# Optimization experiments

Measured on AMD Instinct MI355X. Metric: run time of the kernel, lower is better.

## Reference

```python
import jax, jax.numpy as jnp
import numpy as np

LRELU = 0.2
EPS_LN = 1e-5
EPS_BN = 1e-5


def _seg_softmax(logits, seg, n):
    # softmax over edges grouped by destination node (PyG softmax), logits [E,H]
    m = jax.ops.segment_max(logits, seg, num_segments=n)
    e = jnp.exp(logits - m[seg])
    s = jax.ops.segment_sum(e, seg, num_segments=n)
    return e / (s[seg] + 1e-16)


def _gat(x, src, dst, n, W, a_src, a_dst, b, H, C):
    # PyG GATConv, concat=False (mean over heads), leaky_relu slope 0.2
    h = (x @ W).reshape(n, H, C)
    e = (h * a_src).sum(-1)[src] + (h * a_dst).sum(-1)[dst]  # [E,H]
    e = jnp.where(e > 0, e, LRELU * e)
    alpha = _seg_softmax(e, dst, n)
    out = jax.ops.segment_sum(h[src] * alpha[:, :, None], dst, num_segments=n)  # [N,H,C]
    return out.mean(1) + b


def _gcn(x, src, dst, n, W, b):
    # PyG GCNConv with symmetric normalization; edge list already contains self loops
    deg = jax.ops.segment_sum(jnp.ones(src.shape, x.dtype), dst, num_segments=n)
    dis = jnp.where(deg > 0, jax.lax.rsqrt(jnp.maximum(deg, 1e-12)), 0.0)
    h = x @ W
    w = (dis[src] * dis[dst])[:, None]
    return jax.ops.segment_sum(h[src] * w, dst, num_segments=n) + b


def _ln(x, g, b):
    mu = x.mean(-1, keepdims=True)
    v = x.var(-1, keepdims=True)
    return (x - mu) * jax.lax.rsqrt(v + EPS_LN) * g + b


def _bn_eval(x, g, b, rm, rv):
    return (x - rm) * jax.lax.rsqrt(rv + EPS_BN) * g + b


def _forward(x, edge_index, gin, bti, rmi, rvi, W1, as1, ad1, b1, Wg1, bg1,
             W2, as2, ad2, b2, Wg2, bg2, Ws, bs, Wf, bf,
             g1, be1, g2, be2, g3, be3, Wc1, bc1, gbn, bbn, rmb, rvb, Wc2, bc2):
    n = x.shape[0]
    xn = _bn_eval(x, gin, bti, rmi, rvi)
    sl = jnp.arange(n, dtype=edge_index.dtype)
    src = jnp.concatenate([edge_index[0], sl])
    dst = jnp.concatenate([edge_index[1], sl])
    # GAT1 (4 heads, 128) -> LN -> relu
    x1 = _gat(xn, src, dst, n, W1, as1, ad1, b1, 4, 128)
    x1 = jax.nn.relu(_ln(x1, g1, be1))
    # GCN1 -> relu
    x1g = jax.nn.relu(_gcn(x1, src, dst, n, Wg1, bg1))
    # GAT2 (2 heads, 64) -> LN -> relu
    x2 = _gat(x1g, src, dst, n, W2, as2, ad2, b2, 2, 64)
    x2 = jax.nn.relu(_ln(x2, g2, be2))
    # GCN2 -> relu
    x2g = jax.nn.relu(_gcn(x2, src, dst, n, Wg2, bg2))
    # skip + fusion
    skip = jax.nn.relu(xn @ Ws + bs)
    fused = jax.nn.relu(jnp.concatenate([x1g, x2g], axis=1) @ Wf + bf)
    final = _ln(fused + skip, g3, be3)
    # classifier: Linear -> BN(eval) -> relu -> Linear
    h = jax.nn.relu(_bn_eval(final @ Wc1 + bc1, gbn, bbn, rmb, rvb))
    return h @ Wc2 + bc2


def setup_inputs():
    key = jax.random.key(0)
    ks = jax.random.split(key, 20)
    N, F, E = 20000, 512, 160000
    H1, C1, H2, C2 = 4, 128, 2, 64
    rn = lambda k, sh, s=0.05: (jax.random.normal(k, sh) * s).astype(jnp.float32)
    return dict(
        x=jax.random.normal(ks[0], (N, F), jnp.float32),
        edge_index=jax.random.randint(ks[1], (2, E), 0, N, jnp.int32),
        gin=jnp.ones((F,), jnp.float32), bti=jnp.zeros((F,), jnp.float32),
        rmi=rn(ks[2], (F,)), rvi=(jax.random.uniform(ks[3], (F,)) + 0.5).astype(jnp.float32),
        W1=rn(ks[4], (F, H1 * C1)), as1=rn(ks[5], (H1, C1)), ad1=rn(ks[6], (H1, C1)), b1=jnp.zeros((C1,), jnp.float32),
        Wg1=rn(ks[7], (C1, C1)), bg1=jnp.zeros((C1,), jnp.float32),
        W2=rn(ks[8], (C1, H2 * C2)), as2=rn(ks[9], (H2, C2)), ad2=rn(ks[10], (H2, C2)), b2=jnp.zeros((C2,), jnp.float32),
        Wg2=rn(ks[11], (C2, C2)), bg2=jnp.zeros((C2,), jnp.float32),
        Ws=rn(ks[12], (F, C2)), bs=jnp.zeros((C2,), jnp.float32),
        Wf=rn(ks[13], (C1 + C2, C2)), bf=jnp.zeros((C2,), jnp.float32),
        g1=jnp.ones((C1,), jnp.float32), be1=jnp.zeros((C1,), jnp.float32),
        g2=jnp.ones((C2,), jnp.float32), be2=jnp.zeros((C2,), jnp.float32),
        g3=jnp.ones((C2,), jnp.float32), be3=jnp.zeros((C2,), jnp.float32),
        Wc1=rn(ks[14], (C2, 32)), bc1=jnp.zeros((32,), jnp.float32),
        gbn=jnp.ones((32,), jnp.float32), bbn=jnp.zeros((32,), jnp.float32),
        rmb=rn(ks[15], (32,)), rvb=(jax.random.uniform(ks[16], (32,)) + 0.5).astype(jnp.float32),
        Wc2=rn(ks[17], (32, 5)), bc2=jnp.zeros((5,), jnp.float32),
    )


def reference(x, edge_index, gin, bti, rmi, rvi, W1, as1, ad1, b1, Wg1, bg1,
              W2, as2, ad2, b2, Wg2, bg2, Ws, bs, Wf, bf,
              g1, be1, g2, be2, g3, be3, Wc1, bc1, gbn, bbn, rmb, rvb, Wc2, bc2):
    return _forward(x, edge_index, gin, bti, rmi, rvi, W1, as1, ad1, b1, Wg1, bg1,
                    W2, as2, ad2, b2, Wg2, bg2, Ws, bs, Wf, bf,
                    g1, be1, g2, be2, g3, be3, Wc1, bc1, gbn, bbn, rmb, rvb, Wc2, bc2)
```

## Files before the change

kernel.cpp:

```cpp
#include <hip/hip_runtime.h>
#include <hip/hip_bf16.h>

#define N_NODES 20000
#define F_IN 512

typedef __attribute__((ext_vector_type(8))) short short8;
typedef __attribute__((ext_vector_type(4))) float f32x4;

__device__ __forceinline__ ushort f2bf(float f) {
    uint u = __float_as_uint(f);
    u += 0x7FFF + ((u >> 16) & 1);
    return (ushort)(u >> 16);
}
__device__ __forceinline__ float bf2f(ushort h) { return __uint_as_float((uint)h << 16); }

__device__ __forceinline__ void gload_lds16(const void* g, void* l) {
    __builtin_amdgcn_global_load_lds(
        (const __attribute__((address_space(1))) void*)g,
        (__attribute__((address_space(3))) void*)l, 16, 0, 0);
}

__global__ void zero_int_k(int* p, int n) {
    int i = blockIdx.x * blockDim.x + threadIdx.x;
    if (i < n) p[i] = 0;
}

__global__ void hist_k(const int* __restrict__ ei, int E0, int N, int* __restrict__ deg) {
    int e = blockIdx.x * blockDim.x + threadIdx.x;
    int Etot = E0 + N;
    if (e >= Etot) return;
    int dst = (e < E0) ? ei[E0 + e] : (e - E0);
    atomicAdd(&deg[dst], 1);
}

__global__ __launch_bounds__(1024) void scan_k(const int* __restrict__ deg, int* __restrict__ rp,
                                               int* __restrict__ fp, float* __restrict__ dis,
                                               int N, int Etot) {
    __shared__ int part[1024];
    int tid = threadIdx.x;
    int chunk = (N + 1023) / 1024;
    int lo = tid * chunk, hi = min(lo + chunk, N);
    int s = 0;
    for (int i = lo; i < hi; i++) s += deg[i];
    part[tid] = s;
    __syncthreads();
    for (int off = 1; off < 1024; off <<= 1) {
        int t = 0;
        if (tid >= off) t = part[tid - off];
        __syncthreads();
        part[tid] += t;
        __syncthreads();
    }
    int run = part[tid] - s;
    for (int i = lo; i < hi; i++) {
        rp[i] = run; fp[i] = run;
        int d = deg[i];
        dis[i] = (d > 0) ? rsqrtf((float)d) : 0.f;
        run += d;
    }
    if (tid == 1023) { rp[N] = Etot; fp[N] = Etot; }
}

__global__ void scatter_k(const int* __restrict__ ei, int E0, int N, int* __restrict__ fp,
                          int* __restrict__ csr_src) {
    int e = blockIdx.x * blockDim.x + threadIdx.x;
    int Etot = E0 + N;
    if (e >= Etot) return;
    int src, dst;
    if (e < E0) { src = ei[e]; dst = ei[E0 + e]; }
    else        { src = e - E0; dst = src; }
    int pos = atomicAdd(&fp[dst], 1);
    csr_src[pos] = src;
}

__global__ void bnprep_k(const float* __restrict__ g, const float* __restrict__ b,
                         const float* __restrict__ rm, const float* __restrict__ rv,
                         float* __restrict__ sc, float* __restrict__ sh, int n) {
    int i = blockIdx.x * blockDim.x + threadIdx.x;
    if (i >= n) return;
    float s = g[i] * rsqrtf(rv[i] + 1e-5f);
    sc[i] = s;
    sh[i] = b[i] - rm[i] * s;
}

__global__ void splitA_k(const float* __restrict__ x, const float* __restrict__ sc,
                         const float* __restrict__ sh, ushort* __restrict__ Ah,
                         ushort* __restrict__ Al, int M, int Mpad) {
    size_t i4 = (size_t)blockIdx.x * blockDim.x + threadIdx.x;
    size_t base = i4 * 4;
    if (base >= (size_t)Mpad * 512) return;
    int row = (int)(base >> 9);
    ushort4 ah = {0, 0, 0, 0}, al = {0, 0, 0, 0};
    if (row < M) {
        float4 v = *(const float4*)&x[base];
        int c = (int)(base & 511);
        float f0 = v.x * sc[c] + sh[c];
        float f1 = v.y * sc[c + 1] + sh[c + 1];
        float f2 = v.z * sc[c + 2] + sh[c + 2];
        float f3 = v.w * sc[c + 3] + sh[c + 3];
        ah.x = f2bf(f0); al.x = f2bf(f0 - bf2f(ah.x));
        ah.y = f2bf(f1); al.y = f2bf(f1 - bf2f(ah.y));
        ah.z = f2bf(f2); al.z = f2bf(f2 - bf2f(ah.z));
        ah.w = f2bf(f3); al.w = f2bf(f3 - bf2f(ah.w));
    }
    *(ushort4*)&Ah[base] = ah;
    *(ushort4*)&Al[base] = al;
}

__global__ __launch_bounds__(256) void splitBt_k(const float* __restrict__ W1, const float* __restrict__ Ws,
                                                 ushort* __restrict__ Bth, ushort* __restrict__ Btl) {
    __shared__ float tile[64][65];
    int n0 = blockIdx.x * 64;
    int k0 = blockIdx.y * 64;
    int t = threadIdx.x;
    int a = t >> 6, b = t & 63;
#pragma unroll
    for (int i = 0; i < 16; i++) {
        int kk = a + i * 4, nn = b;
        int gk = k0 + kk, gn = n0 + nn;
        float v;
        if (gn < 512)      v = W1[(size_t)gk * 512 + gn];
        else if (gn < 576) v = Ws[(size_t)gk * 64 + (gn - 512)];
        else               v = 0.f;
        tile[kk][nn] = v;
    }
    __syncthreads();
#pragma unroll
    for (int i = 0; i < 16; i++) {
        int nn = a + i * 4, kk = b;
        float v = tile[kk][nn];
        ushort hi = f2bf(v);
        ushort lo = f2bf(v - bf2f(hi));
        Bth[(size_t)(n0 + nn) * 512 + k0 + kk] = hi;
        Btl[(size_t)(n0 + nn) * 512 + k0 + kk] = lo;
    }
}

__global__ __launch_bounds__(256) void mfma_gemm_k(
    const ushort* __restrict__ Ah, const ushort* __restrict__ Al,
    const ushort* __restrict__ Bth, const ushort* __restrict__ Btl,
    const float* __restrict__ bs, float* __restrict__ h1, float* __restrict__ skip,
    int M, int K) {
    __shared__ ushort Ah_s[128 * 32];
    __shared__ ushort Al_s[128 * 32];
    __shared__ ushort Bh_s[128 * 32];
    __shared__ ushort Bl_s[128 * 32];
    int t = threadIdx.x;
    int w = t >> 6, l = t & 63;
    int bm = blockIdx.y * 128;
    int n0 = blockIdx.x * 128;
    int r0 = (w & 1) * 64, c0 = (w >> 1) * 64;

    f32x4 acc[4][4] = {};

    int elem0 = t * 8;
    int rowS = elem0 >> 5, kofs = elem0 & 31;
    const size_t aoff1 = (size_t)(bm + rowS) * 512 + kofs;
    const size_t aoff2 = (size_t)(bm + rowS + 64) * 512 + kofs;
    const size_t boff1 = (size_t)(n0 + rowS) * 512 + kofs;
    const size_t boff2 = (size_t)(n0 + rowS + 64) * 512 + kofs;

    for (int kt = 0; kt < K; kt += 32) {
        gload_lds16(Ah + aoff1 + kt, &Ah_s[elem0]);
        gload_lds16(Ah + aoff2 + kt, &Ah_s[elem0 + 2048]);
        gload_lds16(Al + aoff1 + kt, &Al_s[elem0]);
        gload_lds16(Al + aoff2 + kt, &Al_s[elem0 + 2048]);
        gload_lds16(Bth + boff1 + kt, &Bh_s[elem0]);
        gload_lds16(Bth + boff2 + kt, &Bh_s[elem0 + 2048]);
        gload_lds16(Btl + boff1 + kt, &Bl_s[elem0]);
        gload_lds16(Btl + boff2 + kt, &Bl_s[elem0 + 2048]);
        __syncthreads();

        short8 ah[4], al4[4], bh[4], bl[4];
        int kg = (l >> 4) * 8;
        int lr = l & 15;
#pragma unroll
        for (int f = 0; f < 4; f++) {
            int ra = (r0 + f * 16 + lr) * 32 + kg;
            ah[f]  = *(const short8*)&Ah_s[ra];
            al4[f] = *(const short8*)&Al_s[ra];
            int rb = (c0 + f * 16 + lr) * 32 + kg;
            bh[f] = *(const short8*)&Bh_s[rb];
            bl[f] = *(const short8*)&Bl_s[rb];
        }
#pragma unroll
        for (int fm = 0; fm < 4; fm++)
#pragma unroll
            for (int fn = 0; fn < 4; fn++) {
                acc[fm][fn] = __builtin_amdgcn_mfma_f32_16x16x32_bf16(ah[fm], bh[fn], acc[fm][fn], 0, 0, 0);
                acc[fm][fn] = __builtin_amdgcn_mfma_f32_16x16x32_bf16(ah[fm], bl[fn], acc[fm][fn], 0, 0, 0);
                acc[fm][fn] = __builtin_amdgcn_mfma_f32_16x16x32_bf16(al4[fm], bh[fn], acc[fm][fn], 0, 0, 0);
            }
        __syncthreads();
    }

#pragma unroll
    for (int fm = 0; fm < 4; fm++) {
        int row_base = bm + r0 + fm * 16 + (l >> 4) * 4;
#pragma unroll
        for (int fn = 0; fn < 4; fn++) {
            int col = n0 + c0 + fn * 16 + (l & 15);
#pragma unroll
            for (int r = 0; r < 4; r++) {
                int row = row_base + r;
                if (row < M) {
                    float v = acc[fm][fn][r];
                    if (col < 512) h1[(size_t)row * 512 + col] = v;
                    else if (col < 576) skip[(size_t)row * 64 + (col - 512)] = fmaxf(v + bs[col - 512], 0.f);
                }
            }
        }
    }
}

template <int K, int NOUT>
__global__ __launch_bounds__(NOUT) void rowgemm_k(const float* __restrict__ X, const float* __restrict__ W,
                                                  float* __restrict__ out, int N) {
    __shared__ float Ws[K * NOUT];
    __shared__ float Xs[4][K];
    int c = threadIdx.x;
    for (int i = c; i < K * NOUT; i += NOUT) Ws[i] = W[i];
    for (int r0 = blockIdx.x * 4; r0 < N; r0 += gridDim.x * 4) {
        int nr = min(4, N - r0);
        __syncthreads();
        for (int i = c; i < nr * K; i += NOUT) Xs[i / K][i % K] = X[(size_t)r0 * K + i];
        __syncthreads();
        float acc[4] = {0.f, 0.f, 0.f, 0.f};
        for (int k = 0; k < K; k++) {
            float w = Ws[k * NOUT + c];
#pragma unroll
            for (int r = 0; r < 4; r++) acc[r] += Xs[r][k] * w;
        }
        for (int r = 0; r < nr; r++) out[(size_t)(r0 + r) * NOUT + c] = acc[r];
    }
}

template <int H, int C>
__global__ __launch_bounds__(256) void scores_k(const float* __restrict__ h, const float* __restrict__ a_src,
                                                const float* __restrict__ a_dst, float* __restrict__ ss,
                                                float* __restrict__ sd, int N) {
    int wid = (blockIdx.x * blockDim.x + threadIdx.x) >> 6;
    int lane = threadIdx.x & 63;
    if (wid >= N * H) return;
    int hh = wid % H;
    const float* hp = h + (size_t)(wid / H) * (H * C) + hh * C;
    float s1 = 0.f, s2 = 0.f;
    for (int c = lane; c < C; c += 64) {
        float v = hp[c];
        s1 += v * a_src[hh * C + c];
        s2 += v * a_dst[hh * C + c];
    }
#pragma unroll
    for (int off = 32; off; off >>= 1) {
        s1 += __shfl_down(s1, off);
        s2 += __shfl_down(s2, off);
    }
    if (lane == 0) { ss[wid] = s1; sd[wid] = s2; }
}

template <int H, int C>
__global__ __launch_bounds__(C) void gat_agg_k(const float* __restrict__ h, const float* __restrict__ ss,
                                               const float* __restrict__ sd, const float* __restrict__ bias,
                                               const float* __restrict__ g, const float* __restrict__ be,
                                               const int* __restrict__ rp, const int* __restrict__ csr_src,
                                               float* __restrict__ out, int N) {
    int n = blockIdx.x;
    int tid = threadIdx.x;
    __shared__ float m_s[H], s_s[H];
    __shared__ int srcs[64];
    __shared__ float aw[64 * H];
    int e0 = rp[n], deg = rp[n + 1] - e0;

    if (tid < H) {
        float m = -1e30f, s = 0.f;
        float sdv = sd[n * H + tid];
        for (int k = 0; k < deg; k++) {
            int src = csr_src[e0 + k];
            float e = ss[src * H + tid] + sdv;
            e = (e > 0.f) ? e : 0.2f * e;
            float mn = fmaxf(m, e);
            s = s * __expf(m - mn) + __expf(e - mn);
            m = mn;
        }
        m_s[tid] = m;
        s_s[tid] = s + 1e-16f;
    }
    __syncthreads();

    float acc = 0.f;
    for (int t0 = 0; t0 < deg; t0 += 64) {
        int tl = min(64, deg - t0);
        if (tid < tl) srcs[tid] = csr_src[e0 + t0 + tid];
        __syncthreads();
        for (int idx = tid; idx < tl * H; idx += C) {
            int k = idx / H, hh = idx % H;
            int src = srcs[k];
            float e = ss[src * H + hh] + sd[n * H + hh];
            e = (e > 0.f) ? e : 0.2f * e;
            aw[idx] = __expf(e - m_s[hh]) / s_s[hh];
        }
        __syncthreads();
        for (int k = 0; k < tl; k++) {
            const float* hp = h + (size_t)srcs[k] * (H * C) + tid;
#pragma unroll
            for (int hh = 0; hh < H; hh++) acc += aw[k * H + hh] * hp[hh * C];
        }
        __syncthreads();
    }

    float v = acc * (1.f / H) + bias[tid];
    float* r1 = aw;
    r1[tid] = v;
    __syncthreads();
    for (int s = C / 2; s > 0; s >>= 1) {
        if (tid < s) r1[tid] += r1[tid + s];
        __syncthreads();
    }
    float mu = r1[0] * (1.f / C);
    __syncthreads();
    float d = v - mu;
    r1[tid] = d * d;
    __syncthreads();
    for (int s = C / 2; s > 0; s >>= 1) {
        if (tid < s) r1[tid] += r1[tid + s];
        __syncthreads();
    }
    float var = r1[0] * (1.f / C);
    float y = d * rsqrtf(var + 1e-5f) * g[tid] + be[tid];
    out[(size_t)n * C + tid] = fmaxf(y, 0.f);
}

template <int C>
__global__ __launch_bounds__(C) void gcn_agg_k(const float* __restrict__ h, const float* __restrict__ dis,
                                               const float* __restrict__ bias, const int* __restrict__ rp,
                                               const int* __restrict__ csr_src, float* __restrict__ out, int N) {
    int n = blockIdx.x;
    int tid = threadIdx.x;
    __shared__ int srcs[64];
    __shared__ float w[64];
    int e0 = rp[n], deg = rp[n + 1] - e0;
    float dn = dis[n];
    float acc = 0.f;
    for (int t0 = 0; t0 < deg; t0 += 64) {
        int tl = min(64, deg - t0);
        if (tid < tl) {
            int s = csr_src[e0 + t0 + tid];
            srcs[tid] = s;
            w[tid] = dis[s] * dn;
        }
        __syncthreads();
        for (int k = 0; k < tl; k++) acc += w[k] * h[(size_t)srcs[k] * C + tid];
        __syncthreads();
    }
    out[(size_t)n * C + tid] = fmaxf(acc + bias[tid], 0.f);
}

__global__ __launch_bounds__(64) void fusion_k(const float* __restrict__ x1g, const float* __restrict__ x2g,
                                               const float* __restrict__ Wf, const float* __restrict__ bf,
                                               const float* __restrict__ skip, const float* __restrict__ g3,
                                               const float* __restrict__ be3, float* __restrict__ fin, int N) {
    int n = blockIdx.x;
    int c = threadIdx.x;
    __shared__ float cat[192];
    cat[c] = x1g[(size_t)n * 128 + c];
    cat[64 + c] = x1g[(size_t)n * 128 + 64 + c];
    cat[128 + c] = x2g[(size_t)n * 64 + c];
    __syncthreads();
    float acc = bf[c];
    for (int j = 0; j < 192; j++) acc += cat[j] * Wf[j * 64 + c];
    acc = fmaxf(acc, 0.f) + skip[(size_t)n * 64 + c];
    float mu = acc;
#pragma unroll
    for (int off = 32; off; off >>= 1) mu += __shfl_xor(mu, off);
    mu *= (1.f / 64.f);
    float d = acc - mu;
    float var = d * d;
#pragma unroll
    for (int off = 32; off; off >>= 1) var += __shfl_xor(var, off);
    var *= (1.f / 64.f);
    fin[(size_t)n * 64 + c] = d * rsqrtf(var + 1e-5f) * g3[c] + be3[c];
}

__global__ __launch_bounds__(64) void classifier_k(const float* __restrict__ fin, const float* __restrict__ Wc1,
                                                   const float* __restrict__ bc1, const float* __restrict__ gbn,
                                                   const float* __restrict__ bbn, const float* __restrict__ rmb,
                                                   const float* __restrict__ rvb, const float* __restrict__ Wc2,
                                                   const float* __restrict__ bc2, float* __restrict__ out, int N) {
    int n = blockIdx.x;
    int t = threadIdx.x;
    __shared__ float f[64];
    __shared__ float hbuf[32];
    f[t] = fin[(size_t)n * 64 + t];
    __syncthreads();
    if (t < 32) {
        float acc = bc1[t];
        for (int j = 0; j < 64; j++) acc += f[j] * Wc1[j * 32 + t];
        acc = (acc - rmb[t]) * rsqrtf(rvb[t] + 1e-5f) * gbn[t] + bbn[t];
        hbuf[t] = fmaxf(acc, 0.f);
    }
    __syncthreads();
    if (t < 5) {
        float acc = bc2[t];
        for (int j = 0; j < 32; j++) acc += hbuf[j] * Wc2[j * 5 + t];
        out[(size_t)n * 5 + t] = acc;
    }
}

extern "C" void kernel_launch(void* const* d_in, const int* in_sizes, int n_in,
                              void* d_out, int out_size, void* d_ws, size_t ws_size,
                              hipStream_t stream) {
    const float* x   = (const float*)d_in[0];
    const int*   ei  = (const int*)d_in[1];
    const float* gin = (const float*)d_in[2];
    const float* bti = (const float*)d_in[3];
    const float* rmi = (const float*)d_in[4];
    const float* rvi = (const float*)d_in[5];
    const float* W1  = (const float*)d_in[6];
    const float* as1 = (const float*)d_in[7];
    const float* ad1 = (const float*)d_in[8];
    const float* b1  = (const float*)d_in[9];
    const float* Wg1 = (const float*)d_in[10];
    const float* bg1 = (const float*)d_in[11];
    const float* W2  = (const float*)d_in[12];
    const float* as2 = (const float*)d_in[13];
    const float* ad2 = (const float*)d_in[14];
    const float* b2  = (const float*)d_in[15];
    const float* Wg2 = (const float*)d_in[16];
    const float* bg2 = (const float*)d_in[17];
    const float* Ws  = (const float*)d_in[18];
    const float* bs  = (const float*)d_in[19];
    const float* Wf  = (const float*)d_in[20];
    const float* bf  = (const float*)d_in[21];
    const float* g1  = (const float*)d_in[22];
    const float* be1 = (const float*)d_in[23];
    const float* g2  = (const float*)d_in[24];
    const float* be2 = (const float*)d_in[25];
    const float* g3  = (const float*)d_in[26];
    const float* be3 = (const float*)d_in[27];
    const float* Wc1 = (const float*)d_in[28];
    const float* bc1 = (const float*)d_in[29];
    const float* gbn = (const float*)d_in[30];
    const float* bbn = (const float*)d_in[31];
    const float* rmb = (const float*)d_in[32];
    const float* rvb = (const float*)d_in[33];
    const float* Wc2 = (const float*)d_in[34];
    const float* bc2 = (const float*)d_in[35];
    float* out = (float*)d_out;

    const int N = in_sizes[0] / F_IN;
    const int E0 = in_sizes[1] / 2;
    const int Etot = E0 + N;
    const int Mpad = 20096;

    char* wp = (char*)d_ws;
    auto alloc = [&](size_t bytes) -> void* {
        void* p = (void*)wp;
        wp += (bytes + 255) & ~(size_t)255;
        return p;
    };
    float* h1   = (float*)alloc((size_t)N * 512 * 4);
    ushort* Ah  = (ushort*)alloc((size_t)Mpad * 512 * 2);
    ushort* Al  = (ushort*)alloc((size_t)Mpad * 512 * 2);
    ushort* Bth = (ushort*)alloc((size_t)640 * 512 * 2);
    ushort* Btl = (ushort*)alloc((size_t)640 * 512 * 2);
    float* skip = (float*)alloc((size_t)N * 64 * 4);
    float* ss1  = (float*)alloc((size_t)N * 4 * 4);
    float* sd1  = (float*)alloc((size_t)N * 4 * 4);
    float* ss2  = (float*)alloc((size_t)N * 2 * 4);
    float* sd2  = (float*)alloc((size_t)N * 2 * 4);
    float* dis  = (float*)alloc((size_t)N * 4);
    float* sc   = (float*)alloc((size_t)F_IN * 4);
    float* sh   = (float*)alloc((size_t)F_IN * 4);
    int* deg    = (int*)alloc((size_t)N * 4);
    int* rp     = (int*)alloc((size_t)(N + 1) * 4);
    int* fp     = (int*)alloc((size_t)(N + 1) * 4);
    int* csr    = (int*)alloc((size_t)Etot * 4);
    float* hg1 = h1;
    float* x1g = h1 + (size_t)N * 128;
    float* h2  = h1 + (size_t)N * 256;
    float* x2  = h1 + (size_t)N * 384;
    float* hg2 = h1 + (size_t)N * 448;
    float* x1  = (float*)Ah;
    float* x2g = x1 + (size_t)N * 128;
    float* fin = x2g + (size_t)N * 64;

    zero_int_k<<<(N + 255) / 256, 256, 0, stream>>>(deg, N);
    hist_k<<<(Etot + 255) / 256, 256, 0, stream>>>(ei, E0, N, deg);
    scan_k<<<1, 1024, 0, stream>>>(deg, rp, fp, dis, N, Etot);
    scatter_k<<<(Etot + 255) / 256, 256, 0, stream>>>(ei, E0, N, fp, csr);
    bnprep_k<<<2, 256, 0, stream>>>(gin, bti, rmi, rvi, sc, sh, F_IN);
    splitA_k<<<(int)(((size_t)Mpad * 512 / 4 + 255) / 256), 256, 0, stream>>>(x, sc, sh, Ah, Al, N, Mpad);
    splitBt_k<<<dim3(10, 8), 256, 0, stream>>>(W1, Ws, Bth, Btl);

    mfma_gemm_k<<<dim3(5, 157), 256, 0, stream>>>(Ah, Al, Bth, Btl, bs, h1, skip, N, 512);

    scores_k<4, 128><<<(N * 4 + 3) / 4, 256, 0, stream>>>(h1, as1, ad1, ss1, sd1, N);
    gat_agg_k<4, 128><<<N, 128, 0, stream>>>(h1, ss1, sd1, b1, g1, be1, rp, csr, x1, N);

    rowgemm_k<128, 128><<<512, 128, 0, stream>>>(x1, Wg1, hg1, N);
    gcn_agg_k<128><<<N, 128, 0, stream>>>(hg1, dis, bg1, rp, csr, x1g, N);

    rowgemm_k<128, 128><<<512, 128, 0, stream>>>(x1g, W2, h2, N);
    scores_k<2, 64><<<(N * 2 + 3) / 4, 256, 0, stream>>>(h2, as2, ad2, ss2, sd2, N);
    gat_agg_k<2, 64><<<N, 64, 0, stream>>>(h2, ss2, sd2, b2, g2, be2, rp, csr, x2, N);

    rowgemm_k<64, 64><<<512, 64, 0, stream>>>(x2, Wg2, hg2, N);
    gcn_agg_k<64><<<N, 64, 0, stream>>>(hg2, dis, bg2, rp, csr, x2g, N);

    fusion_k<<<N, 64, 0, stream>>>(x1g, x2g, Wf, bf, skip, g3, be3, fin, N);

    classifier_k<<<N, 64, 0, stream>>>(fin, Wc1, bc1, gbn, bbn, rmb, rvb, Wc2, bc2, out, N);
}
```

Measured before the change: 583.8 us.

## Remap GEMM grid across XCDs, parallelize GAT softmax, fuse tail kernels

Several independent changes land together. The MFMA GEMM now uses a 1D grid that is remapped so neighbouring tiles land on the same XCD, and its LDS layout moves to k-group-major. rowgemm processes 8 rows per block and is launched on more blocks. GAT aggregation computes the online softmax with 32 lanes per head instead of one thread per head, caches edge logits in shared memory for small degrees, and does the LayerNorm with shuffles instead of a shared-memory tree. The final GCN aggregation, fusion and classifier are merged into one kernel, which removes intermediate buffers and launches but puts more work in each block.

```diff
diff --git a/kernel.cpp b/kernel.cpp
--- a/kernel.cpp
+++ b/kernel.cpp
@@ -147,39 +147,46 @@
     __shared__ ushort Bl_s[128 * 32];
     int t = threadIdx.x;
     int w = t >> 6, l = t & 63;
-    int bm = blockIdx.y * 128;
-    int n0 = blockIdx.x * 128;
+
+    int nwg = gridDim.x;
+    int q = nwg >> 3, r = nwg & 7;
+    int xcd = blockIdx.x & 7, lid = blockIdx.x >> 3;
+    int wg = (xcd < r) ? xcd * (q + 1) + lid : r * (q + 1) + (xcd - r) * q + lid;
+    int by = wg / 5, bx = wg % 5;
+    int bm = by * 128;
+    int n0 = bx * 128;
     int r0 = (w & 1) * 64, c0 = (w >> 1) * 64;
 
     f32x4 acc[4][4] = {};
 
+    int kg_t = t >> 7;
+    int row_t = t & 127;
+    const size_t ga1 = (size_t)(bm + row_t) * 512 + kg_t * 8;
+    const size_t ga2 = (size_t)(bm + row_t) * 512 + (kg_t + 2) * 8;
+    const size_t gb1 = (size_t)(n0 + row_t) * 512 + kg_t * 8;
+    const size_t gb2 = (size_t)(n0 + row_t) * 512 + (kg_t + 2) * 8;
     int elem0 = t * 8;
-    int rowS = elem0 >> 5, kofs = elem0 & 31;
-    const size_t aoff1 = (size_t)(bm + rowS) * 512 + kofs;
-    const size_t aoff2 = (size_t)(bm + rowS + 64) * 512 + kofs;
-    const size_t boff1 = (size_t)(n0 + rowS) * 512 + kofs;
-    const size_t boff2 = (size_t)(n0 + rowS + 64) * 512 + kofs;
 
     for (int kt = 0; kt < K; kt += 32) {
-        gload_lds16(Ah + aoff1 + kt, &Ah_s[elem0]);
-        gload_lds16(Ah + aoff2 + kt, &Ah_s[elem0 + 2048]);
-        gload_lds16(Al + aoff1 + kt, &Al_s[elem0]);
-        gload_lds16(Al + aoff2 + kt, &Al_s[elem0 + 2048]);
-        gload_lds16(Bth + boff1 + kt, &Bh_s[elem0]);
-        gload_lds16(Bth + boff2 + kt, &Bh_s[elem0 + 2048]);
-        gload_lds16(Btl + boff1 + kt, &Bl_s[elem0]);
-        gload_lds16(Btl + boff2 + kt, &Bl_s[elem0 + 2048]);
+        gload_lds16(Ah + ga1 + kt, &Ah_s[elem0]);
+        gload_lds16(Ah + ga2 + kt, &Ah_s[elem0 + 2048]);
+        gload_lds16(Al + ga1 + kt, &Al_s[elem0]);
+        gload_lds16(Al + ga2 + kt, &Al_s[elem0 + 2048]);
+        gload_lds16(Bth + gb1 + kt, &Bh_s[elem0]);
+        gload_lds16(Bth + gb2 + kt, &Bh_s[elem0 + 2048]);
+        gload_lds16(Btl + gb1 + kt, &Bl_s[elem0]);
+        gload_lds16(Btl + gb2 + kt, &Bl_s[elem0 + 2048]);
         __syncthreads();
 
         short8 ah[4], al4[4], bh[4], bl[4];
-        int kg = (l >> 4) * 8;
+        int kgl = l >> 4;
         int lr = l & 15;
 #pragma unroll
         for (int f = 0; f < 4; f++) {
-            int ra = (r0 + f * 16 + lr) * 32 + kg;
+            int ra = kgl * 1024 + (r0 + f * 16 + lr) * 8;
             ah[f]  = *(const short8*)&Ah_s[ra];
             al4[f] = *(const short8*)&Al_s[ra];
-            int rb = (c0 + f * 16 + lr) * 32 + kg;
+            int rb = kgl * 1024 + (c0 + f * 16 + lr) * 8;
             bh[f] = *(const short8*)&Bh_s[rb];
             bl[f] = *(const short8*)&Bl_s[rb];
         }
@@ -201,10 +208,10 @@
         for (int fn = 0; fn < 4; fn++) {
             int col = n0 + c0 + fn * 16 + (l & 15);
 #pragma unroll
-            for (int r = 0; r < 4; r++) {
-                int row = row_base + r;
+            for (int r2 = 0; r2 < 4; r2++) {
+                int row = row_base + r2;
                 if (row < M) {
-                    float v = acc[fm][fn][r];
+                    float v = acc[fm][fn][r2];
                     if (col < 512) h1[(size_t)row * 512 + col] = v;
                     else if (col < 576) skip[(size_t)row * 64 + (col - 512)] = fmaxf(v + bs[col - 512], 0.f);
                 }
@@ -217,19 +224,19 @@
 __global__ __launch_bounds__(NOUT) void rowgemm_k(const float* __restrict__ X, const float* __restrict__ W,
                                                   float* __restrict__ out, int N) {
     __shared__ float Ws[K * NOUT];
-    __shared__ float Xs[4][K];
+    __shared__ float Xs[8][K];
     int c = threadIdx.x;
     for (int i = c; i < K * NOUT; i += NOUT) Ws[i] = W[i];
-    for (int r0 = blockIdx.x * 4; r0 < N; r0 += gridDim.x * 4) {
-        int nr = min(4, N - r0);
+    for (int r0 = blockIdx.x * 8; r0 < N; r0 += gridDim.x * 8) {
+        int nr = min(8, N - r0);
         __syncthreads();
         for (int i = c; i < nr * K; i += NOUT) Xs[i / K][i % K] = X[(size_t)r0 * K + i];
         __syncthreads();
-        float acc[4] = {0.f, 0.f, 0.f, 0.f};
+        float acc[8] = {};
         for (int k = 0; k < K; k++) {
             float w = Ws[k * NOUT + c];
 #pragma unroll
-            for (int r = 0; r < 4; r++) acc[r] += Xs[r][k] * w;
+            for (int r = 0; r < 8; r++) acc[r] += Xs[r][k] * w;
         }
         for (int r = 0; r < nr; r++) out[(size_t)(r0 + r) * NOUT + c] = acc[r];
     }
@@ -266,66 +273,94 @@
                                                float* __restrict__ out, int N) {
     int n = blockIdx.x;
     int tid = threadIdx.x;
-    __shared__ float m_s[H], s_s[H];
+    __shared__ float m_s[H], s_s[H], red[4];
     __shared__ int srcs[64];
     __shared__ float aw[64 * H];
     int e0 = rp[n], deg = rp[n + 1] - e0;
-
-    if (tid < H) {
-        float m = -1e30f, s = 0.f;
-        float sdv = sd[n * H + tid];
+    bool small = (deg <= 64);
+    int hh = tid >> 5, l = tid & 31;
+
+    if (small && tid < deg) srcs[tid] = csr_src[e0 + tid];
+    __syncthreads();
+
+    float sdv = sd[n * H + hh];
+    float m = -1e30f, s = 0.f;
+    for (int k = l; k < deg; k += 32) {
+        int src = small ? srcs[k] : csr_src[e0 + k];
+        float e = ss[src * H + hh] + sdv;
+        e = (e > 0.f) ? e : 0.2f * e;
+        if (small) aw[k * H + hh] = e;
+        float mn = fmaxf(m, e);
+        s = s * __expf(m - mn) + __expf(e - mn);
+        m = mn;
+    }
+#pragma unroll
+    for (int off = 16; off; off >>= 1) {
+        float mo = __shfl_xor(m, off), so = __shfl_xor(s, off);
+        float mn = fmaxf(m, mo);
+        s = s * __expf(m - mn) + so * __expf(mo - mn);
+        m = mn;
+    }
+    if (l == 0) { m_s[hh] = m; s_s[hh] = s + 1e-16f; }
+    __syncthreads();
+
+    float v = 0.f;
+    if (small) {
+        for (int idx = tid; idx < deg * H; idx += C) {
+            int h2 = idx & (H - 1);
+            aw[idx] = __expf(aw[idx] - m_s[h2]) / s_s[h2];
+        }
+        __syncthreads();
         for (int k = 0; k < deg; k++) {
-            int src = csr_src[e0 + k];
-            float e = ss[src * H + tid] + sdv;
-            e = (e > 0.f) ? e : 0.2f * e;
-            float mn = fmaxf(m, e);
-            s = s * __expf(m - mn) + __expf(e - mn);
-            m = mn;
-        }
-        m_s[tid] = m;
-        s_s[tid] = s + 1e-16f;
-    }
-    __syncthreads();
-
-    float acc = 0.f;
-    for (int t0 = 0; t0 < deg; t0 += 64) {
-        int tl = min(64, deg - t0);
-        if (tid < tl) srcs[tid] = csr_src[e0 + t0 + tid];
-        __syncthreads();
-        for (int idx = tid; idx < tl * H; idx += C) {
-            int k = idx / H, hh = idx % H;
-            int src = srcs[k];
-            float e = ss[src * H + hh] + sd[n * H + hh];
-            e = (e > 0.f) ? e : 0.2f * e;
-            aw[idx] = __expf(e - m_s[hh]) / s_s[hh];
-        }
-        __syncthreads();
-        for (int k = 0; k < tl; k++) {
             const float* hp = h + (size_t)srcs[k] * (H * C) + tid;
 #pragma unroll
-            for (int hh = 0; hh < H; hh++) acc += aw[k * H + hh] * hp[hh * C];
-        }
-        __syncthreads();
-    }
-
-    float v = acc * (1.f / H) + bias[tid];
-    float* r1 = aw;
-    r1[tid] = v;
-    __syncthreads();
-    for (int s = C / 2; s > 0; s >>= 1) {
-        if (tid < s) r1[tid] += r1[tid + s];
-        __syncthreads();
-    }
-    float mu = r1[0] * (1.f / C);
-    __syncthreads();
+            for (int h2 = 0; h2 < H; h2++) v += aw[k * H + h2] * hp[h2 * C];
+        }
+    } else {
+        for (int t0 = 0; t0 < deg; t0 += 64) {
+            int tl = min(64, deg - t0);
+            __syncthreads();
+            if (tid < tl) srcs[tid] = csr_src[e0 + t0 + tid];
+            __syncthreads();
+            for (int idx = tid; idx < tl * H; idx += C) {
+                int k = idx / H, h2 = idx & (H - 1);
+                float e = ss[srcs[k] * H + h2] + sd[n * H + h2];
+                e = (e > 0.f) ? e : 0.2f * e;
+                aw[idx] = __expf(e - m_s[h2]) / s_s[h2];
+            }
+            __syncthreads();
+            for (int k = 0; k < tl; k++) {
+                const float* hp = h + (size_t)srcs[k] * (H * C) + tid;
+#pragma unroll
+                for (int h2 = 0; h2 < H; h2++) v += aw[k * H + h2] * hp[h2 * C];
+            }
+        }
+    }
+
+    v = v * (1.f / H) + bias[tid];
+    float t1 = v;
+#pragma unroll
+    for (int off = 32; off; off >>= 1) t1 += __shfl_xor(t1, off);
+    float mu;
+    if (C == 128) {
+        if ((tid & 63) == 0) red[tid >> 6] = t1;
+        __syncthreads();
+        mu = (red[0] + red[1]) * (1.f / C);
+    } else {
+        mu = t1 * (1.f / C);
+    }
     float d = v - mu;
-    r1[tid] = d * d;
-    __syncthreads();
-    for (int s = C / 2; s > 0; s >>= 1) {
-        if (tid < s) r1[tid] += r1[tid + s];
-        __syncthreads();
-    }
-    float var = r1[0] * (1.f / C);
+    float t2 = d * d;
+#pragma unroll
+    for (int off = 32; off; off >>= 1) t2 += __shfl_xor(t2, off);
+    float var;
+    if (C == 128) {
+        if ((tid & 63) == 0) red[2 + (tid >> 6)] = t2;
+        __syncthreads();
+        var = (red[2] + red[3]) * (1.f / C);
+    } else {
+        var = t2 * (1.f / C);
+    }
     float y = d * rsqrtf(var + 1e-5f) * g[tid] + be[tid];
     out[(size_t)n * C + tid] = fmaxf(y, 0.f);
 }
@@ -355,54 +390,65 @@
     out[(size_t)n * C + tid] = fmaxf(acc + bias[tid], 0.f);
 }
 
-__global__ __launch_bounds__(64) void fusion_k(const float* __restrict__ x1g, const float* __restrict__ x2g,
-                                               const float* __restrict__ Wf, const float* __restrict__ bf,
-                                               const float* __restrict__ skip, const float* __restrict__ g3,
-                                               const float* __restrict__ be3, float* __restrict__ fin, int N) {
+__global__ __launch_bounds__(64) void final_fused_k(
+    const float* __restrict__ hg2, const float* __restrict__ dis, const float* __restrict__ bg2,
+    const int* __restrict__ rp, const int* __restrict__ csr_src,
+    const float* __restrict__ x1g, const float* __restrict__ Wf, const float* __restrict__ bf,
+    const float* __restrict__ skip, const float* __restrict__ g3, const float* __restrict__ be3,
+    const float* __restrict__ Wc1, const float* __restrict__ bc1, const float* __restrict__ gbn,
+    const float* __restrict__ bbn, const float* __restrict__ rmb, const float* __restrict__ rvb,
+    const float* __restrict__ Wc2, const float* __restrict__ bc2, float* __restrict__ out, int N) {
     int n = blockIdx.x;
-    int c = threadIdx.x;
+    int tid = threadIdx.x;
+    __shared__ int srcs[64];
+    __shared__ float w[64];
     __shared__ float cat[192];
-    cat[c] = x1g[(size_t)n * 128 + c];
-    cat[64 + c] = x1g[(size_t)n * 128 + 64 + c];
-    cat[128 + c] = x2g[(size_t)n * 64 + c];
-    __syncthreads();
-    float acc = bf[c];
-    for (int j = 0; j < 192; j++) acc += cat[j] * Wf[j * 64 + c];
-    acc = fmaxf(acc, 0.f) + skip[(size_t)n * 64 + c];
-    float mu = acc;
-#pragma unroll
-    for (int off = 32; off; off >>= 1) mu += __shfl_xor(mu, off);
-    mu *= (1.f / 64.f);
-    float d = acc - mu;
-    float var = d * d;
-#pragma unroll
-    for (int off = 32; off; off >>= 1) var += __shfl_xor(var, off);
-    var *= (1.f / 64.f);
-    fin[(size_t)n * 64 + c] = d * rsqrtf(var + 1e-5f) * g3[c] + be3[c];
-}
-
-__global__ __launch_bounds__(64) void classifier_k(const float* __restrict__ fin, const float* __restrict__ Wc1,
-                                                   const float* __restrict__ bc1, const float* __restrict__ gbn,
-                                                   const float* __restrict__ bbn, const float* __restrict__ rmb,
-                                                   const float* __restrict__ rvb, const float* __restrict__ Wc2,
-                                                   const float* __restrict__ bc2, float* __restrict__ out, int N) {
-    int n = blockIdx.x;
-    int t = threadIdx.x;
-    __shared__ float f[64];
+    __shared__ float fbuf[64];
     __shared__ float hbuf[32];
-    f[t] = fin[(size_t)n * 64 + t];
-    __syncthreads();
-    if (t < 32) {
-        float acc = bc1[t];
-        for (int j = 0; j < 64; j++) acc += f[j] * Wc1[j * 32 + t];
-        acc = (acc - rmb[t]) * rsqrtf(rvb[t] + 1e-5f) * gbn[t] + bbn[t];
-        hbuf[t] = fmaxf(acc, 0.f);
-    }
-    __syncthreads();
-    if (t < 5) {
-        float acc = bc2[t];
-        for (int j = 0; j < 32; j++) acc += hbuf[j] * Wc2[j * 5 + t];
-        out[(size_t)n * 5 + t] = acc;
+    int e0 = rp[n], deg = rp[n + 1] - e0;
+    float dn = dis[n];
+    float acc = 0.f;
+    for (int t0 = 0; t0 < deg; t0 += 64) {
+        int tl = min(64, deg - t0);
+        if (tid < tl) {
+            int s = csr_src[e0 + t0 + tid];
+            srcs[tid] = s;
+            w[tid] = dis[s] * dn;
+        }
+        __syncthreads();
+        for (int k = 0; k < tl; k++) acc += w[k] * hg2[(size_t)srcs[k] * 64 + tid];
+        __syncthreads();
+    }
+    float x2gv = fmaxf(acc + bg2[tid], 0.f);
+    cat[tid] = x1g[(size_t)n * 128 + tid];
+    cat[64 + tid] = x1g[(size_t)n * 128 + 64 + tid];
+    cat[128 + tid] = x2gv;
+    __syncthreads();
+    float fa = bf[tid];
+    for (int j = 0; j < 192; j++) fa += cat[j] * Wf[j * 64 + tid];
+    fa = fmaxf(fa, 0.f) + skip[(size_t)n * 64 + tid];
+    float t1 = fa;
+#pragma unroll
+    for (int off = 32; off; off >>= 1) t1 += __shfl_xor(t1, off);
+    float mu = t1 * (1.f / 64.f);
+    float d = fa - mu;
+    float t2 = d * d;
+#pragma unroll
+    for (int off = 32; off; off >>= 1) t2 += __shfl_xor(t2, off);
+    float var = t2 * (1.f / 64.f);
+    fbuf[tid] = d * rsqrtf(var + 1e-5f) * g3[tid] + be3[tid];
+    __syncthreads();
+    if (tid < 32) {
+        float a = bc1[tid];
+        for (int j = 0; j < 64; j++) a += fbuf[j] * Wc1[j * 32 + tid];
+        a = (a - rmb[tid]) * rsqrtf(rvb[tid] + 1e-5f) * gbn[tid] + bbn[tid];
+        hbuf[tid] = fmaxf(a, 0.f);
+    }
+    __syncthreads();
+    if (tid < 5) {
+        float a = bc2[tid];
+        for (int j = 0; j < 32; j++) a += hbuf[j] * Wc2[j * 5 + tid];
+        out[(size_t)n * 5 + tid] = a;
     }
 }
 
@@ -481,8 +527,6 @@
     float* x2  = h1 + (size_t)N * 384;
     float* hg2 = h1 + (size_t)N * 448;
     float* x1  = (float*)Ah;
-    float* x2g = x1 + (size_t)N * 128;
-    float* fin = x2g + (size_t)N * 64;
 
     zero_int_k<<<(N + 255) / 256, 256, 0, stream>>>(deg, N);
     hist_k<<<(Etot + 255) / 256, 256, 0, stream>>>(ei, E0, N, deg);
@@ -492,22 +536,20 @@
     splitA_k<<<(int)(((size_t)Mpad * 512 / 4 + 255) / 256), 256, 0, stream>>>(x, sc, sh, Ah, Al, N, Mpad);
     splitBt_k<<<dim3(10, 8), 256, 0, stream>>>(W1, Ws, Bth, Btl);
 
-    mfma_gemm_k<<<dim3(5, 157), 256, 0, stream>>>(Ah, Al, Bth, Btl, bs, h1, skip, N, 512);
+    mfma_gemm_k<<<785, 256, 0, stream>>>(Ah, Al, Bth, Btl, bs, h1, skip, N, 512);
 
     scores_k<4, 128><<<(N * 4 + 3) / 4, 256, 0, stream>>>(h1, as1, ad1, ss1, sd1, N);
     gat_agg_k<4, 128><<<N, 128, 0, stream>>>(h1, ss1, sd1, b1, g1, be1, rp, csr, x1, N);
 
-    rowgemm_k<128, 128><<<512, 128, 0, stream>>>(x1, Wg1, hg1, N);
+    rowgemm_k<128, 128><<<1280, 128, 0, stream>>>(x1, Wg1, hg1, N);
     gcn_agg_k<128><<<N, 128, 0, stream>>>(hg1, dis, bg1, rp, csr, x1g, N);
 
-    rowgemm_k<128, 128><<<512, 128, 0, stream>>>(x1g, W2, h2, N);
+    rowgemm_k<128, 128><<<1280, 128, 0, stream>>>(x1g, W2, h2, N);
     scores_k<2, 64><<<(N * 2 + 3) / 4, 256, 0, stream>>>(h2, as2, ad2, ss2, sd2, N);
     gat_agg_k<2, 64><<<N, 64, 0, stream>>>(h2, ss2, sd2, b2, g2, be2, rp, csr, x2, N);
 
-    rowgemm_k<64, 64><<<512, 64, 0, stream>>>(x2, Wg2, hg2, N);
-    gcn_agg_k<64><<<N, 64, 0, stream>>>(hg2, dis, bg2, rp, csr, x2g, N);
-
-    fusion_k<<<N, 64, 0, stream>>>(x1g, x2g, Wf, bf, skip, g3, be3, fin, N);
-
-    classifier_k<<<N, 64, 0, stream>>>(fin, Wc1, bc1, gbn, bbn, rmb, rvb, Wc2, bc2, out, N);
-}
+    rowgemm_k<64, 64><<<1280, 64, 0, stream>>>(x2, Wg2, hg2, N);
+
+    final_fused_k<<<N, 64, 0, stream>>>(hg2, dis, bg2, rp, csr, x1g, Wf, bf, skip, g3, be3,
+                                        Wc1, bc1, gbn, bbn, rmb, rvb, Wc2, bc2, out, N);
+}
```

Measured after the change: 577.1 us. About the same (-1.1%).
